# Kernel optimization log

Hardware: AMD Instinct MI355X
Metric: run time of the kernel (lower is better)

The kernel has to match this reference:

```python
import jax, jax.numpy as jnp
import numpy as np

NUM_HEADS = 16
EPS = 1e-6
CHUNK = 128  # chunk length for exact chunked-recurrent causal linear attention


def setup_inputs() -> dict:
    key = jax.random.key(0)
    ks = jax.random.split(key, 6)
    B, T, E = 4, 2048, 1024
    s = 0.02
    x = jax.random.normal(ks[0], (B, T, E), jnp.float32)
    Wq = jax.random.normal(ks[1], (E, E), jnp.float32) * s
    Wk = jax.random.normal(ks[2], (E, E), jnp.float32) * s
    Wv = jax.random.normal(ks[3], (E, E), jnp.float32) * s
    Wp = jax.random.normal(ks[4], (E, E), jnp.float32) * s
    bp = jnp.zeros((E,), jnp.float32)
    return {"x": x, "Wq": Wq, "Wk": Wk, "Wv": Wv, "Wp": Wp, "bp": bp}


def reference(x, Wq, Wk, Wv, Wp, bp):
    B, T, E = x.shape
    H = NUM_HEADS
    D = E // H
    N = T // CHUNK

    q = x @ Wq.T
    k = x @ Wk.T
    v = x @ Wv.T

    def split_heads(t):  # [B,T,E] -> [B,H,N,C,D]
        return t.reshape(B, T, H, D).transpose(0, 2, 1, 3).reshape(B, H, N, CHUNK, D)

    phi_q = jax.nn.elu(split_heads(q)) + 1.0
    phi_k = jax.nn.elu(split_heads(k)) + 1.0
    vh = split_heads(v)

    # per-chunk KV state and key-sum, then exclusive prefix over chunks
    kv = jnp.einsum('bhncd,bhnce->bhnde', phi_k, vh)        # [B,H,N,D,D]
    zk = phi_k.sum(axis=3)                                   # [B,H,N,D]
    S_prev = jnp.concatenate(
        [jnp.zeros_like(kv[:, :, :1]), jnp.cumsum(kv, axis=2)[:, :, :-1]], axis=2)
    Z_prev = jnp.concatenate(
        [jnp.zeros_like(zk[:, :, :1]), jnp.cumsum(zk, axis=2)[:, :, :-1]], axis=2)

    # intra-chunk causal part
    A = jnp.einsum('bhncd,bhnsd->bhncs', phi_q, phi_k)       # [B,H,N,C,C]
    mask = jnp.tril(jnp.ones((CHUNK, CHUNK), bool))
    A = jnp.where(mask, A, 0.0)

    num = (jnp.einsum('bhncs,bhnse->bhnce', A, vh)
           + jnp.einsum('bhncd,bhnde->bhnce', phi_q, S_prev))
    den = A.sum(-1) + jnp.einsum('bhncd,bhnd->bhnc', phi_q, Z_prev) + EPS
    y = num / den[..., None]                                  # [B,H,N,C,D]

    y = y.reshape(B, H, T, D).transpose(0, 2, 1, 3).reshape(B, T, E)
    return y @ Wp.T + bp
```

## Files before the change

### kernel.cpp

```cpp
#include <hip/hip_runtime.h>
#include <hip/hip_bf16.h>
#include <stdint.h>

#define T_LEN  2048
#define E_DIM  1024
#define BATCH  4
#define HEADS  16
#define HDIM   64
#define CHUNK_ 128
#define NCHUNK 16
#define EPS_   1e-6f

typedef __attribute__((ext_vector_type(8))) short bf16x8;
typedef __attribute__((ext_vector_type(4))) float f32x4;

__device__ __forceinline__ float b2f(__hip_bfloat16 h) { return __bfloat162float(h); }
__device__ __forceinline__ unsigned short f2bu(float f) {
  __hip_bfloat16 h = __float2bfloat16(f);
  return *(unsigned short*)&h;
}
__device__ __forceinline__ float bs2f(short v) {
  union { unsigned int u; float f; } c;
  c.u = ((unsigned int)(unsigned short)v) << 16;
  return c.f;
}
__device__ __forceinline__ void gld_lds16(const void* g, void* l) {
  __builtin_amdgcn_global_load_lds((const __attribute__((address_space(1))) void*)g,
                                   (__attribute__((address_space(3))) void*)l,
                                   16, 0, 0);
}

__global__ __launch_bounds__(256)
void cast5(const float* __restrict__ x,  const float* __restrict__ w0,
           const float* __restrict__ w1, const float* __restrict__ w2,
           const float* __restrict__ w3,
           __hip_bfloat16* __restrict__ xb,  __hip_bfloat16* __restrict__ w0b,
           __hip_bfloat16* __restrict__ w1b, __hip_bfloat16* __restrict__ w2b,
           __hip_bfloat16* __restrict__ w3b)
{
  const int b = blockIdx.x;
  const float* s;
  __hip_bfloat16* d;
  size_t off;
  if (b < 8192) { s = x; d = xb; off = (size_t)b * 1024; }
  else {
    const int i = (b - 8192) >> 10;
    const int r = (b - 8192) & 1023;
    s = (i == 0) ? w0 : (i == 1) ? w1 : (i == 2) ? w2 : w3;
    d = (i == 0) ? w0b : (i == 1) ? w1b : (i == 2) ? w2b : w3b;
    off = (size_t)r * 1024;
  }
  const int t = threadIdx.x;
  float4 v = *(const float4*)(s + off + (size_t)t * 4);
  ushort4 o;
  o.x = f2bu(v.x); o.y = f2bu(v.y); o.z = f2bu(v.z); o.w = f2bu(v.w);
  *(ushort4*)((unsigned short*)d + off + (size_t)t * 4) = o;
}

__device__ __forceinline__ void gemm128_core(
    const __hip_bfloat16* __restrict__ X,
    const __hip_bfloat16* __restrict__ W,
    int bm, int bn, f32x4 acc[4][4],
    __hip_bfloat16* Xs, __hip_bfloat16* Ws)
{
  const int t = threadIdx.x, lane = t & 63, wave = t >> 6;
  const int wm = (wave >> 1) * 64, wn = (wave & 1) * 64;
  for (int k0 = 0; k0 < 1024; k0 += 32) {
    if (k0) __syncthreads();
#pragma unroll
    for (int i = 0; i < 2; ++i) {
      const int j = wave * 2 + i;
      const int m = j * 16 + (lane >> 2);
      const int kg = lane & 3;
      gld_lds16(X + (size_t)(bm * 128 + m) * 1024 + k0 + kg * 8, (char*)Xs + j * 1024);
      gld_lds16(W + (size_t)(bn * 128 + m) * 1024 + k0 + kg * 8, (char*)Ws + j * 1024);
    }
    __syncthreads();
    bf16x8 a[4], b[4];
#pragma unroll
    for (int i = 0; i < 4; ++i) {
      a[i] = *(const bf16x8*)&Xs[((wm + i * 16 + (lane & 15)) * 4 + (lane >> 4)) * 8];
      b[i] = *(const bf16x8*)&Ws[((wn + i * 16 + (lane & 15)) * 4 + (lane >> 4)) * 8];
    }
#pragma unroll
    for (int i = 0; i < 4; ++i)
#pragma unroll
      for (int jn = 0; jn < 4; ++jn)
        acc[i][jn] = __builtin_amdgcn_mfma_f32_16x16x32_bf16(a[i], b[jn], acc[i][jn], 0, 0, 0);
  }
}

__global__ __launch_bounds__(256, 2)
void gemm_qkv(const __hip_bfloat16* __restrict__ X,
              const __hip_bfloat16* __restrict__ Wq,
              const __hip_bfloat16* __restrict__ Wk,
              const __hip_bfloat16* __restrict__ Wv,
              __hip_bfloat16* __restrict__ qo,
              __hip_bfloat16* __restrict__ ko,
              __hip_bfloat16* __restrict__ vo)
{
  __shared__ __align__(16) __hip_bfloat16 Xs[128 * 32];
  __shared__ __align__(16) __hip_bfloat16 Ws[128 * 32];
  const int bm = blockIdx.x, bnx = blockIdx.y;
  const int which = bnx >> 3, bn = bnx & 7;
  const __hip_bfloat16* W = (which == 0) ? Wq : (which == 1) ? Wk : Wv;
  __hip_bfloat16* C = (which == 0) ? qo : (which == 1) ? ko : vo;
  const bool elu = (which < 2);
  f32x4 acc[4][4];
#pragma unroll
  for (int i = 0; i < 4; ++i)
#pragma unroll
    for (int j = 0; j < 4; ++j) acc[i][j] = (f32x4){0.f, 0.f, 0.f, 0.f};
  gemm128_core(X, W, bm, bn, acc, Xs, Ws);
  const int lane = threadIdx.x & 63, wave = threadIdx.x >> 6;
  const int wm = (wave >> 1) * 64, wn = (wave & 1) * 64;
  const int r0 = (lane >> 4) * 4;
#pragma unroll
  for (int mi = 0; mi < 4; ++mi)
#pragma unroll
    for (int ni = 0; ni < 4; ++ni) {
      const int row = bm * 128 + wm + mi * 16 + r0;
      const int col = bn * 128 + wn + ni * 16 + (lane & 15);
#pragma unroll
      for (int r = 0; r < 4; ++r) {
        float v = acc[mi][ni][r];
        if (elu) v = (v > 0.f) ? (v + 1.f) : __expf(v);
        C[(size_t)(row + r) * 1024 + col] = __float2bfloat16(v);
      }
    }
}

__global__ __launch_bounds__(256, 2)
void gemm_out(const __hip_bfloat16* __restrict__ X,
              const __hip_bfloat16* __restrict__ W,
              const float* __restrict__ bias,
              float* __restrict__ C)
{
  __shared__ __align__(16) __hip_bfloat16 Xs[128 * 32];
  __shared__ __align__(16) __hip_bfloat16 Ws[128 * 32];
  const int bm = blockIdx.x, bn = blockIdx.y;
  f32x4 acc[4][4];
#pragma unroll
  for (int i = 0; i < 4; ++i)
#pragma unroll
    for (int j = 0; j < 4; ++j) acc[i][j] = (f32x4){0.f, 0.f, 0.f, 0.f};
  gemm128_core(X, W, bm, bn, acc, Xs, Ws);
  const int lane = threadIdx.x & 63, wave = threadIdx.x >> 6;
  const int wm = (wave >> 1) * 64, wn = (wave & 1) * 64;
  const int r0 = (lane >> 4) * 4;
#pragma unroll
  for (int mi = 0; mi < 4; ++mi)
#pragma unroll
    for (int ni = 0; ni < 4; ++ni) {
      const int row = bm * 128 + wm + mi * 16 + r0;
      const int col = bn * 128 + wn + ni * 16 + (lane & 15);
      const float bv = bias[col];
#pragma unroll
      for (int r = 0; r < 4; ++r)
        C[(size_t)(row + r) * 1024 + col] = acc[mi][ni][r] + bv;
    }
}

__global__ __launch_bounds__(256)
void chunk_kv(const __hip_bfloat16* __restrict__ Kp,
              const __hip_bfloat16* __restrict__ Vp,
              float* __restrict__ kvout, float* __restrict__ zkout)
{
  const int bid = blockIdx.x;
  const int n = bid & 15, h = (bid >> 4) & 15, b = bid >> 8;
  __shared__ __align__(16) __hip_bfloat16 ks[CHUNK_ * HDIM];
  __shared__ __align__(16) __hip_bfloat16 vs[CHUNK_ * HDIM];
  const size_t base = ((size_t)(b * T_LEN + n * CHUNK_)) * E_DIM + h * HDIM;
  const int t = threadIdx.x;
  for (int i = t; i < CHUNK_ * 8; i += 256) {
    int r = i >> 3, c = (i & 7) << 3;
    *(uint4*)&ks[r * HDIM + c] = *(const uint4*)(Kp + base + (size_t)r * E_DIM + c);
    *(uint4*)&vs[r * HDIM + c] = *(const uint4*)(Vp + base + (size_t)r * E_DIM + c);
  }
  __syncthreads();
  const int d0 = (t >> 4) << 2, e0 = (t & 15) << 2;
  float acc[4][4] = {{0.f}};
  float z[4] = {0.f, 0.f, 0.f, 0.f};
  for (int c = 0; c < CHUNK_; ++c) {
    float kv4[4], vv4[4];
#pragma unroll
    for (int i = 0; i < 4; ++i) kv4[i] = b2f(ks[c * HDIM + d0 + i]);
#pragma unroll
    for (int j = 0; j < 4; ++j) vv4[j] = b2f(vs[c * HDIM + e0 + j]);
#pragma unroll
    for (int i = 0; i < 4; ++i) {
      z[i] += kv4[i];
#pragma unroll
      for (int j = 0; j < 4; ++j) acc[i][j] += kv4[i] * vv4[j];
    }
  }
  float* o = kvout + (size_t)bid * (HDIM * HDIM);
#pragma unroll
  for (int i = 0; i < 4; ++i)
#pragma unroll
    for (int j = 0; j < 4; ++j)
      o[(e0 + j) * HDIM + (d0 + i)] = acc[i][j];
  if (e0 == 0) {
#pragma unroll
    for (int i = 0; i < 4; ++i) zkout[(size_t)bid * HDIM + d0 + i] = z[i];
  }
}

__global__ __launch_bounds__(256)
void prefix_chunks(float* __restrict__ S, float* __restrict__ Z)
{
  const int bh = blockIdx.x;
  const int t = threadIdx.x;
  float run[16];
#pragma unroll
  for (int j = 0; j < 16; ++j) run[j] = 0.f;
  for (int n = 0; n < NCHUNK; ++n) {
    float* p = S + ((size_t)bh * NCHUNK + n) * (HDIM * HDIM);
#pragma unroll
    for (int j = 0; j < 16; ++j) {
      int idx = t + j * 256;
      float cur = p[idx];
      p[idx] = run[j];
      run[j] += cur;
    }
  }
  if (t < HDIM) {
    float rz = 0.f;
    for (int n = 0; n < NCHUNK; ++n) {
      float* p = Z + ((size_t)bh * NCHUNK + n) * HDIM + t;
      float cur = *p;
      *p = rz;
      rz += cur;
    }
  }
}

__global__ __launch_bounds__(256, 2)
void chunk_attn(const __hip_bfloat16* __restrict__ Qp,
                const __hip_bfloat16* __restrict__ Kp,
                const __hip_bfloat16* __restrict__ Vp,
                const float* __restrict__ STp,
                const float* __restrict__ Zp,
                __hip_bfloat16* __restrict__ Yp)
{
  __shared__ __align__(16) __hip_bfloat16 QK[16384];
  __shared__ __align__(16) __hip_bfloat16 Vt[8192];
  __shared__ __align__(16) __hip_bfloat16 Sb[4096];
  __shared__ float den_lds[128];
  __shared__ float Zs[64];

  const int bid = blockIdx.x;
  const int n = bid & 15, h = (bid >> 4) & 15, b = bid >> 8;
  const int tokbase = b * T_LEN + n * CHUNK_;
  const size_t gbase = (size_t)tokbase * E_DIM + h * HDIM;
  const int t = threadIdx.x, lane = t & 63, wv = t >> 6;
  unsigned short* QKu = (unsigned short*)QK;
  short* VtS = (short*)Vt;

#pragma unroll
  for (int i = 0; i < 4; ++i) {
    const int m = i * 32 + (t >> 3);
    const int d0 = (t & 7) << 3;
    uint4 qv = *(const uint4*)(Qp + gbase + (size_t)m * E_DIM + d0);
    uint4 kv = *(const uint4*)(Kp + gbase + (size_t)m * E_DIM + d0);
    *(uint4*)&QK[((d0 >> 3) * 128 + m) * 8] = qv;
    *(uint4*)&QK[8192 + ((d0 >> 3) * 128 + m) * 8] = kv;
  }
#pragma unroll
  for (int i = 0; i < 4; ++i) {
    const int j = wv * 4 + i;
    const int slot = j * 64 + lane;
    const int s = slot >> 3, e8 = slot & 7;
    gld_lds16(Vp + gbase + (size_t)s * E_DIM + e8 * 8, (char*)Vt + j * 1024);
  }
  {
    const float* Sg = STp + (size_t)bid * (HDIM * HDIM);
    const int e = t >> 2, quad = t & 3;
#pragma unroll
    for (int i = 0; i < 4; ++i) {
      const int d0 = quad * 16 + i * 4;
      float4 sv = *(const float4*)(Sg + e * HDIM + d0);
      ushort4 o;
      o.x = f2bu(sv.x); o.y = f2bu(sv.y); o.z = f2bu(sv.z); o.w = f2bu(sv.w);
      *(ushort4*)&QKu[0] ;
      *(ushort4*)&((unsigned short*)Sb)[((d0 >> 3) * 64 + e) * 8 + (d0 & 7)] = o;
    }
  }
  if (t < 64) Zs[t] = Zp[(size_t)bid * HDIM + t];
  __syncthreads();

  const int mts[2] = { wv, 7 - wv };
  f32x4 accn[2][4];
#pragma unroll
  for (int i = 0; i < 2; ++i)
#pragma unroll
    for (int j = 0; j < 4; ++j) accn[i][j] = (f32x4){0.f, 0.f, 0.f, 0.f};

#pragma unroll
  for (int mi = 0; mi < 2; ++mi) {
    const int m0 = mts[mi] * 16;
#pragma unroll
    for (int kh = 0; kh < 2; ++kh) {
      bf16x8 a = *(const bf16x8*)&QK[(((kh * 4) + (lane >> 4)) * 128 + m0 + (lane & 15)) * 8];
#pragma unroll
      for (int ne = 0; ne < 4; ++ne) {
        bf16x8 bsf = *(const bf16x8*)&Sb[(((kh * 4) + (lane >> 4)) * 64 + ne * 16 + (lane & 15)) * 8];
        accn[mi][ne] = __builtin_amdgcn_mfma_f32_16x16x32_bf16(a, bsf, accn[mi][ne], 0, 0, 0);
      }
    }
  }
  if (t < 128) {
    float dn = EPS_;
#pragma unroll
    for (int kg = 0; kg < 8; ++kg) {
      bf16x8 qv = *(const bf16x8*)&QK[(kg * 128 + t) * 8];
#pragma unroll
      for (int j = 0; j < 8; ++j) dn += bs2f(qv[j]) * Zs[kg * 8 + j];
    }
    den_lds[t] = dn;
  }
  uint2 packP[9];
  {
    int np = 0;
#pragma unroll
    for (int mi = 0; mi < 2; ++mi) {
      const int mt = mts[mi], m0 = mt * 16;
      bf16x8 aq0 = *(const bf16x8*)&QK[(((lane >> 4)) * 128 + m0 + (lane & 15)) * 8];
      bf16x8 aq1 = *(const bf16x8*)&QK[((4 + (lane >> 4)) * 128 + m0 + (lane & 15)) * 8];
      for (int nt = 0; nt <= mt; ++nt) {
        f32x4 acc = (f32x4){0.f, 0.f, 0.f, 0.f};
        bf16x8 b0 = *(const bf16x8*)&QK[8192 + (((lane >> 4)) * 128 + nt * 16 + (lane & 15)) * 8];
        bf16x8 b1 = *(const bf16x8*)&QK[8192 + ((4 + (lane >> 4)) * 128 + nt * 16 + (lane & 15)) * 8];
        acc = __builtin_amdgcn_mfma_f32_16x16x32_bf16(aq0, b0, acc, 0, 0, 0);
        acc = __builtin_amdgcn_mfma_f32_16x16x32_bf16(aq1, b1, acc, 0, 0, 0);
        unsigned short u[4];
#pragma unroll
        for (int r = 0; r < 4; ++r) {
          float v = acc[r];
          if (nt == mt) {
            const bool keep = (lane & 15) <= (((lane >> 4) * 4) + r);
            v = keep ? v : 0.f;
          }
          u[r] = f2bu(v);
        }
        packP[np].x = (unsigned)u[0] | ((unsigned)u[1] << 16);
        packP[np].y = (unsigned)u[2] | ((unsigned)u[3] << 16);
        ++np;
      }
    }
  }
  __syncthreads();

  {
    int np = 0;
#pragma unroll
    for (int mi = 0; mi < 2; ++mi) {
      const int mt = mts[mi], m0 = mt * 16;
      for (int nt = 0; nt <= mt; ++nt) {
        const uint2 p = packP[np++];
        const int s = nt * 16 + (lane & 15);
        const int kgs = s >> 3, se = s & 7;
#pragma unroll
        for (int r = 0; r < 4; ++r) {
          const int m = m0 + (lane >> 4) * 4 + r;
          unsigned short us = (r < 2) ? (unsigned short)(p.x >> (r * 16))
                                      : (unsigned short)(p.y >> ((r - 2) * 16));
          QKu[(kgs * 128 + m) * 8 + se] = us;
        }
      }
      if ((mt & 1) == 0 && lane < 32) {
        const int slot = (2 * mt + 2 + (lane >> 4)) * 128 + m0 + (lane & 15);
        *(uint4*)&QK[slot * 8] = (uint4){0u, 0u, 0u, 0u};
      }
    }
  }
  __syncthreads();

  bf16x8 ones;
#pragma unroll
  for (int j = 0; j < 8; ++j) ones[j] = (short)0x3F80;
  f32x4 accden[2];
  accden[0] = (f32x4){0.f, 0.f, 0.f, 0.f};
  accden[1] = (f32x4){0.f, 0.f, 0.f, 0.f};
#pragma unroll
  for (int mi = 0; mi < 2; ++mi) {
    const int mt = mts[mi], m0 = mt * 16;
    const int ktc = (mt + 2) >> 1;
    for (int kt = 0; kt < ktc; ++kt) {
      bf16x8 a = *(const bf16x8*)&QK[((kt * 4 + (lane >> 4)) * 128 + m0 + (lane & 15)) * 8];
      accden[mi] = __builtin_amdgcn_mfma_f32_16x16x32_bf16(a, ones, accden[mi], 0, 0, 0);
#pragma unroll
      for (int ne = 0; ne < 4; ++ne) {
        bf16x8 bv;
#pragma unroll
        for (int j = 0; j < 8; ++j)
          bv[j] = VtS[(kt * 32 + (lane >> 4) * 8 + j) * 64 + ne * 16 + (lane & 15)];
        accn[mi][ne] = __builtin_amdgcn_mfma_f32_16x16x32_bf16(a, bv, accn[mi][ne], 0, 0, 0);
      }
    }
    if ((lane & 15) == 0) {
#pragma unroll
      for (int r = 0; r < 4; ++r)
        den_lds[m0 + (lane >> 4) * 4 + r] += accden[mi][r];
    }
  }
  __syncthreads();

#pragma unroll
  for (int mi = 0; mi < 2; ++mi) {
    const int m0 = mts[mi] * 16;
    float inv[4];
#pragma unroll
    for (int r = 0; r < 4; ++r)
      inv[r] = 1.f / den_lds[m0 + (lane >> 4) * 4 + r];
#pragma unroll
    for (int ne = 0; ne < 4; ++ne) {
      const int col = h * HDIM + ne * 16 + (lane & 15);
#pragma unroll
      for (int r = 0; r < 4; ++r) {
        const int row = tokbase + m0 + (lane >> 4) * 4 + r;
        Yp[(size_t)row * E_DIM + col] = __float2bfloat16(accn[mi][ne][r] * inv[r]);
      }
    }
  }
}

extern "C" void kernel_launch(void* const* d_in, const int* in_sizes, int n_in,
                              void* d_out, int out_size, void* d_ws, size_t ws_size,
                              hipStream_t stream)
{
  const float* x  = (const float*)d_in[0];
  const float* Wq = (const float*)d_in[1];
  const float* Wk = (const float*)d_in[2];
  const float* Wv = (const float*)d_in[3];
  const float* Wp = (const float*)d_in[4];
  const float* bp = (const float*)d_in[5];
  float* out = (float*)d_out;

  const size_t MT = (size_t)BATCH * T_LEN;
  char* w = (char*)d_ws;
  __hip_bfloat16* xb  = (__hip_bfloat16*)w; w += MT * E_DIM * sizeof(__hip_bfloat16);
  __hip_bfloat16* Wqb = (__hip_bfloat16*)w; w += (size_t)E_DIM * E_DIM * sizeof(__hip_bfloat16);
  __hip_bfloat16* Wkb = (__hip_bfloat16*)w; w += (size_t)E_DIM * E_DIM * sizeof(__hip_bfloat16);
  __hip_bfloat16* Wvb = (__hip_bfloat16*)w; w += (size_t)E_DIM * E_DIM * sizeof(__hip_bfloat16);
  __hip_bfloat16* Wpb = (__hip_bfloat16*)w; w += (size_t)E_DIM * E_DIM * sizeof(__hip_bfloat16);
  __hip_bfloat16* q = (__hip_bfloat16*)w; w += MT * E_DIM * sizeof(__hip_bfloat16);
  __hip_bfloat16* k = (__hip_bfloat16*)w; w += MT * E_DIM * sizeof(__hip_bfloat16);
  __hip_bfloat16* v = (__hip_bfloat16*)w; w += MT * E_DIM * sizeof(__hip_bfloat16);
  __hip_bfloat16* y = (__hip_bfloat16*)w; w += MT * E_DIM * sizeof(__hip_bfloat16);
  float* S = (float*)w; w += (size_t)BATCH * HEADS * NCHUNK * HDIM * HDIM * sizeof(float);
  float* Z = (float*)w; w += (size_t)BATCH * HEADS * NCHUNK * HDIM * sizeof(float);

  cast5<<<8192 + 4096, 256, 0, stream>>>(x, Wq, Wk, Wv, Wp, xb, Wqb, Wkb, Wvb, Wpb);
  gemm_qkv<<<dim3(MT / 128, 24), 256, 0, stream>>>(xb, Wqb, Wkb, Wvb, q, k, v);
  chunk_kv<<<BATCH * HEADS * NCHUNK, 256, 0, stream>>>(k, v, S, Z);
  prefix_chunks<<<BATCH * HEADS, 256, 0, stream>>>(S, Z);
  chunk_attn<<<BATCH * HEADS * NCHUNK, 256, 0, stream>>>(q, k, v, S, Z, y);
  gemm_out<<<dim3(MT / 128, 8), 256, 0, stream>>>(y, Wpb, bp, out);
}
```

Baseline: 256.2 us.

## Restructure chunk attention with pre-packed V/S layouts and per-wave P tiles

chunk_kv now writes the KV state directly in the MFMA-friendly blocked layout and also emits a pre-transposed bf16 V image (reusing the xb buffer), so chunk_attn can load V and S with straight vector copies instead of gathering. chunk_attn keeps Q fragments in registers loaded directly from global, computes the denominator with an MFMA against Z, and stores each wave's masked QK^T tile in a private padded LDS region instead of rewriting a shared QK buffer, which removes two block barriers. LDS use shrinks and launch bounds allow three blocks per CU. The cost is that K fragments are now read from global inside the inner loop and chunk_kv does extra transpose writes.

```diff
diff --git a/kernel.cpp b/kernel.cpp
--- a/kernel.cpp
+++ b/kernel.cpp
@@ -18,11 +18,6 @@
 __device__ __forceinline__ unsigned short f2bu(float f) {
   __hip_bfloat16 h = __float2bfloat16(f);
   return *(unsigned short*)&h;
-}
-__device__ __forceinline__ float bs2f(short v) {
-  union { unsigned int u; float f; } c;
-  c.u = ((unsigned int)(unsigned short)v) << 16;
-  return c.f;
 }
 __device__ __forceinline__ void gld_lds16(const void* g, void* l) {
   __builtin_amdgcn_global_load_lds((const __attribute__((address_space(1))) void*)g,
@@ -164,7 +159,8 @@
 __global__ __launch_bounds__(256)
 void chunk_kv(const __hip_bfloat16* __restrict__ Kp,
               const __hip_bfloat16* __restrict__ Vp,
-              float* __restrict__ kvout, float* __restrict__ zkout)
+              float* __restrict__ kvout, float* __restrict__ zkout,
+              unsigned short* __restrict__ vimg)
 {
   const int bid = blockIdx.x;
   const int n = bid & 15, h = (bid >> 4) & 15, b = bid >> 8;
@@ -195,14 +191,27 @@
     }
   }
   float* o = kvout + (size_t)bid * (HDIM * HDIM);
+  const int dg = d0 >> 3, doff = d0 & 7;
 #pragma unroll
   for (int i = 0; i < 4; ++i)
 #pragma unroll
     for (int j = 0; j < 4; ++j)
-      o[(e0 + j) * HDIM + (d0 + i)] = acc[i][j];
+      o[dg * 512 + (e0 + j) * 8 + doff + i] = acc[i][j];
   if (e0 == 0) {
 #pragma unroll
     for (int i = 0; i < 4; ++i) zkout[(size_t)bid * HDIM + d0 + i] = z[i];
+  }
+  const unsigned short* vsu = (const unsigned short*)vs;
+  unsigned short* vo = vimg + (size_t)bid * 8192;
+  for (int slot = t; slot < 1024; slot += 256) {
+    const int sg = slot >> 6, e = slot & 63;
+    ushort4 lo, hi;
+    lo.x = vsu[(sg * 8 + 0) * 64 + e]; lo.y = vsu[(sg * 8 + 1) * 64 + e];
+    lo.z = vsu[(sg * 8 + 2) * 64 + e]; lo.w = vsu[(sg * 8 + 3) * 64 + e];
+    hi.x = vsu[(sg * 8 + 4) * 64 + e]; hi.y = vsu[(sg * 8 + 5) * 64 + e];
+    hi.z = vsu[(sg * 8 + 6) * 64 + e]; hi.w = vsu[(sg * 8 + 7) * 64 + e];
+    *(ushort4*)&vo[slot * 8] = lo;
+    *(ushort4*)&vo[slot * 8 + 4] = hi;
   }
 }
 
@@ -235,190 +244,142 @@
   }
 }
 
-__global__ __launch_bounds__(256, 2)
+#define PW_STRIDE 136
+
+__global__ __launch_bounds__(256, 3)
 void chunk_attn(const __hip_bfloat16* __restrict__ Qp,
                 const __hip_bfloat16* __restrict__ Kp,
-                const __hip_bfloat16* __restrict__ Vp,
-                const float* __restrict__ STp,
+                const unsigned short* __restrict__ vimg,
+                const float* __restrict__ Simg,
                 const float* __restrict__ Zp,
                 __hip_bfloat16* __restrict__ Yp)
 {
-  __shared__ __align__(16) __hip_bfloat16 QK[16384];
-  __shared__ __align__(16) __hip_bfloat16 Vt[8192];
-  __shared__ __align__(16) __hip_bfloat16 Sb[4096];
-  __shared__ float den_lds[128];
-  __shared__ float Zs[64];
+  __shared__ __align__(16) unsigned short VL[8192];
+  __shared__ __align__(16) unsigned short SL[4096];
+  __shared__ __align__(16) unsigned short PL[4 * 16 * PW_STRIDE];
 
   const int bid = blockIdx.x;
   const int n = bid & 15, h = (bid >> 4) & 15, b = bid >> 8;
   const int tokbase = b * T_LEN + n * CHUNK_;
   const size_t gbase = (size_t)tokbase * E_DIM + h * HDIM;
   const int t = threadIdx.x, lane = t & 63, wv = t >> 6;
-  unsigned short* QKu = (unsigned short*)QK;
-  short* VtS = (short*)Vt;
-
-#pragma unroll
-  for (int i = 0; i < 4; ++i) {
-    const int m = i * 32 + (t >> 3);
-    const int d0 = (t & 7) << 3;
-    uint4 qv = *(const uint4*)(Qp + gbase + (size_t)m * E_DIM + d0);
-    uint4 kv = *(const uint4*)(Kp + gbase + (size_t)m * E_DIM + d0);
-    *(uint4*)&QK[((d0 >> 3) * 128 + m) * 8] = qv;
-    *(uint4*)&QK[8192 + ((d0 >> 3) * 128 + m) * 8] = kv;
-  }
+  const int lm = lane & 15, kg = lane >> 4;
+
 #pragma unroll
   for (int i = 0; i < 4; ++i) {
     const int j = wv * 4 + i;
-    const int slot = j * 64 + lane;
-    const int s = slot >> 3, e8 = slot & 7;
-    gld_lds16(Vp + gbase + (size_t)s * E_DIM + e8 * 8, (char*)Vt + j * 1024);
-  }
-  {
-    const float* Sg = STp + (size_t)bid * (HDIM * HDIM);
-    const int e = t >> 2, quad = t & 3;
-#pragma unroll
-    for (int i = 0; i < 4; ++i) {
-      const int d0 = quad * 16 + i * 4;
-      float4 sv = *(const float4*)(Sg + e * HDIM + d0);
-      ushort4 o;
-      o.x = f2bu(sv.x); o.y = f2bu(sv.y); o.z = f2bu(sv.z); o.w = f2bu(sv.w);
-      *(ushort4*)&QKu[0] ;
-      *(ushort4*)&((unsigned short*)Sb)[((d0 >> 3) * 64 + e) * 8 + (d0 & 7)] = o;
-    }
-  }
-  if (t < 64) Zs[t] = Zp[(size_t)bid * HDIM + t];
+    gld_lds16(vimg + (size_t)bid * 8192 + (size_t)(j * 64 + lane) * 8,
+              (char*)VL + j * 1024);
+  }
+#pragma unroll
+  for (int i = 0; i < 4; ++i) {
+    const int idx = i * 1024 + t * 4;
+    float4 s4 = *(const float4*)(Simg + (size_t)bid * 4096 + idx);
+    ushort4 o;
+    o.x = f2bu(s4.x); o.y = f2bu(s4.y); o.z = f2bu(s4.z); o.w = f2bu(s4.w);
+    *(ushort4*)&SL[idx] = o;
+  }
+
+  const int mts[2] = { wv, 7 - wv };
+  bf16x8 aq[2][2];
+#pragma unroll
+  for (int mi = 0; mi < 2; ++mi)
+#pragma unroll
+    for (int kh = 0; kh < 2; ++kh)
+      aq[mi][kh] = *(const bf16x8*)(Qp + gbase +
+                    (size_t)(mts[mi] * 16 + lm) * E_DIM + kh * 32 + kg * 8);
+  bf16x8 zb[2];
+#pragma unroll
+  for (int kh = 0; kh < 2; ++kh) {
+    float4 z0 = *(const float4*)(Zp + (size_t)bid * 64 + kh * 32 + kg * 8);
+    float4 z1 = *(const float4*)(Zp + (size_t)bid * 64 + kh * 32 + kg * 8 + 4);
+    zb[kh][0] = (short)f2bu(z0.x); zb[kh][1] = (short)f2bu(z0.y);
+    zb[kh][2] = (short)f2bu(z0.z); zb[kh][3] = (short)f2bu(z0.w);
+    zb[kh][4] = (short)f2bu(z1.x); zb[kh][5] = (short)f2bu(z1.y);
+    zb[kh][6] = (short)f2bu(z1.z); zb[kh][7] = (short)f2bu(z1.w);
+  }
+
   __syncthreads();
 
-  const int mts[2] = { wv, 7 - wv };
   f32x4 accn[2][4];
-#pragma unroll
-  for (int i = 0; i < 2; ++i)
-#pragma unroll
-    for (int j = 0; j < 4; ++j) accn[i][j] = (f32x4){0.f, 0.f, 0.f, 0.f};
-
+  f32x4 accden[2];
 #pragma unroll
   for (int mi = 0; mi < 2; ++mi) {
-    const int m0 = mts[mi] * 16;
+    accden[mi] = (f32x4){EPS_, EPS_, EPS_, EPS_};
+#pragma unroll
+    for (int ne = 0; ne < 4; ++ne) accn[mi][ne] = (f32x4){0.f, 0.f, 0.f, 0.f};
+  }
+
+#pragma unroll
+  for (int mi = 0; mi < 2; ++mi)
 #pragma unroll
     for (int kh = 0; kh < 2; ++kh) {
-      bf16x8 a = *(const bf16x8*)&QK[(((kh * 4) + (lane >> 4)) * 128 + m0 + (lane & 15)) * 8];
+      const bf16x8 a = aq[mi][kh];
+      accden[mi] = __builtin_amdgcn_mfma_f32_16x16x32_bf16(a, zb[kh], accden[mi], 0, 0, 0);
 #pragma unroll
       for (int ne = 0; ne < 4; ++ne) {
-        bf16x8 bsf = *(const bf16x8*)&Sb[(((kh * 4) + (lane >> 4)) * 64 + ne * 16 + (lane & 15)) * 8];
-        accn[mi][ne] = __builtin_amdgcn_mfma_f32_16x16x32_bf16(a, bsf, accn[mi][ne], 0, 0, 0);
-      }
-    }
-  }
-  if (t < 128) {
-    float dn = EPS_;
-#pragma unroll
-    for (int kg = 0; kg < 8; ++kg) {
-      bf16x8 qv = *(const bf16x8*)&QK[(kg * 128 + t) * 8];
-#pragma unroll
-      for (int j = 0; j < 8; ++j) dn += bs2f(qv[j]) * Zs[kg * 8 + j];
-    }
-    den_lds[t] = dn;
-  }
-  uint2 packP[9];
-  {
-    int np = 0;
-#pragma unroll
-    for (int mi = 0; mi < 2; ++mi) {
-      const int mt = mts[mi], m0 = mt * 16;
-      bf16x8 aq0 = *(const bf16x8*)&QK[(((lane >> 4)) * 128 + m0 + (lane & 15)) * 8];
-      bf16x8 aq1 = *(const bf16x8*)&QK[((4 + (lane >> 4)) * 128 + m0 + (lane & 15)) * 8];
-      for (int nt = 0; nt <= mt; ++nt) {
-        f32x4 acc = (f32x4){0.f, 0.f, 0.f, 0.f};
-        bf16x8 b0 = *(const bf16x8*)&QK[8192 + (((lane >> 4)) * 128 + nt * 16 + (lane & 15)) * 8];
-        bf16x8 b1 = *(const bf16x8*)&QK[8192 + ((4 + (lane >> 4)) * 128 + nt * 16 + (lane & 15)) * 8];
-        acc = __builtin_amdgcn_mfma_f32_16x16x32_bf16(aq0, b0, acc, 0, 0, 0);
-        acc = __builtin_amdgcn_mfma_f32_16x16x32_bf16(aq1, b1, acc, 0, 0, 0);
-        unsigned short u[4];
-#pragma unroll
-        for (int r = 0; r < 4; ++r) {
-          float v = acc[r];
-          if (nt == mt) {
-            const bool keep = (lane & 15) <= (((lane >> 4) * 4) + r);
-            v = keep ? v : 0.f;
-          }
-          u[r] = f2bu(v);
-        }
-        packP[np].x = (unsigned)u[0] | ((unsigned)u[1] << 16);
-        packP[np].y = (unsigned)u[2] | ((unsigned)u[3] << 16);
-        ++np;
-      }
-    }
-  }
-  __syncthreads();
-
-  {
-    int np = 0;
-#pragma unroll
-    for (int mi = 0; mi < 2; ++mi) {
-      const int mt = mts[mi], m0 = mt * 16;
-      for (int nt = 0; nt <= mt; ++nt) {
-        const uint2 p = packP[np++];
-        const int s = nt * 16 + (lane & 15);
-        const int kgs = s >> 3, se = s & 7;
-#pragma unroll
-        for (int r = 0; r < 4; ++r) {
-          const int m = m0 + (lane >> 4) * 4 + r;
-          unsigned short us = (r < 2) ? (unsigned short)(p.x >> (r * 16))
-                                      : (unsigned short)(p.y >> ((r - 2) * 16));
-          QKu[(kgs * 128 + m) * 8 + se] = us;
-        }
-      }
-      if ((mt & 1) == 0 && lane < 32) {
-        const int slot = (2 * mt + 2 + (lane >> 4)) * 128 + m0 + (lane & 15);
-        *(uint4*)&QK[slot * 8] = (uint4){0u, 0u, 0u, 0u};
-      }
-    }
-  }
-  __syncthreads();
-
+        bf16x8 bs = *(const bf16x8*)&SL[((kh * 4 + kg) * 64 + ne * 16 + lm) * 8];
+        accn[mi][ne] = __builtin_amdgcn_mfma_f32_16x16x32_bf16(a, bs, accn[mi][ne], 0, 0, 0);
+      }
+    }
+
+  unsigned short* Pw = PL + wv * 16 * PW_STRIDE;
   bf16x8 ones;
 #pragma unroll
   for (int j = 0; j < 8; ++j) ones[j] = (short)0x3F80;
-  f32x4 accden[2];
-  accden[0] = (f32x4){0.f, 0.f, 0.f, 0.f};
-  accden[1] = (f32x4){0.f, 0.f, 0.f, 0.f};
+
 #pragma unroll
   for (int mi = 0; mi < 2; ++mi) {
     const int mt = mts[mi], m0 = mt * 16;
+    for (int nt = 0; nt <= mt; ++nt) {
+      f32x4 pt = (f32x4){0.f, 0.f, 0.f, 0.f};
+#pragma unroll
+      for (int kh = 0; kh < 2; ++kh) {
+        bf16x8 ak = *(const bf16x8*)(Kp + gbase +
+                     (size_t)(nt * 16 + lm) * E_DIM + kh * 32 + kg * 8);
+        pt = __builtin_amdgcn_mfma_f32_16x16x32_bf16(ak, aq[mi][kh], pt, 0, 0, 0);
+      }
+      unsigned short u[4];
+#pragma unroll
+      for (int r = 0; r < 4; ++r) {
+        float v = pt[r];
+        if (nt == mt) {
+          v = ((kg * 4 + r) <= lm) ? v : 0.f;
+        }
+        u[r] = f2bu(v);
+      }
+      const int sidx = lm * PW_STRIDE + nt * 16 + kg * 4;
+      *(unsigned*)&Pw[sidx]     = (unsigned)u[0] | ((unsigned)u[1] << 16);
+      *(unsigned*)&Pw[sidx + 2] = (unsigned)u[2] | ((unsigned)u[3] << 16);
+    }
+    if ((mt & 1) == 0 && lane < 32) {
+      const int m = lane >> 1, half = lane & 1;
+      *(uint4*)&Pw[m * PW_STRIDE + (mt + 1) * 16 + half * 8] = (uint4){0u, 0u, 0u, 0u};
+    }
     const int ktc = (mt + 2) >> 1;
     for (int kt = 0; kt < ktc; ++kt) {
-      bf16x8 a = *(const bf16x8*)&QK[((kt * 4 + (lane >> 4)) * 128 + m0 + (lane & 15)) * 8];
-      accden[mi] = __builtin_amdgcn_mfma_f32_16x16x32_bf16(a, ones, accden[mi], 0, 0, 0);
+      bf16x8 ap = *(const bf16x8*)&Pw[lm * PW_STRIDE + kt * 32 + kg * 8];
+      accden[mi] = __builtin_amdgcn_mfma_f32_16x16x32_bf16(ap, ones, accden[mi], 0, 0, 0);
 #pragma unroll
       for (int ne = 0; ne < 4; ++ne) {
-        bf16x8 bv;
-#pragma unroll
-        for (int j = 0; j < 8; ++j)
-          bv[j] = VtS[(kt * 32 + (lane >> 4) * 8 + j) * 64 + ne * 16 + (lane & 15)];
-        accn[mi][ne] = __builtin_amdgcn_mfma_f32_16x16x32_bf16(a, bv, accn[mi][ne], 0, 0, 0);
-      }
-    }
-    if ((lane & 15) == 0) {
-#pragma unroll
-      for (int r = 0; r < 4; ++r)
-        den_lds[m0 + (lane >> 4) * 4 + r] += accden[mi][r];
-    }
-  }
-  __syncthreads();
+        bf16x8 bv = *(const bf16x8*)&VL[((kt * 4 + kg) * 64 + ne * 16 + lm) * 8];
+        accn[mi][ne] = __builtin_amdgcn_mfma_f32_16x16x32_bf16(ap, bv, accn[mi][ne], 0, 0, 0);
+      }
+    }
+  }
 
 #pragma unroll
   for (int mi = 0; mi < 2; ++mi) {
     const int m0 = mts[mi] * 16;
     float inv[4];
 #pragma unroll
-    for (int r = 0; r < 4; ++r)
-      inv[r] = 1.f / den_lds[m0 + (lane >> 4) * 4 + r];
+    for (int r = 0; r < 4; ++r) inv[r] = 1.f / accden[mi][r];
 #pragma unroll
     for (int ne = 0; ne < 4; ++ne) {
-      const int col = h * HDIM + ne * 16 + (lane & 15);
+      const int col = h * HDIM + ne * 16 + lm;
 #pragma unroll
       for (int r = 0; r < 4; ++r) {
-        const int row = tokbase + m0 + (lane >> 4) * 4 + r;
+        const int row = tokbase + m0 + kg * 4 + r;
         Yp[(size_t)row * E_DIM + col] = __float2bfloat16(accn[mi][ne][r] * inv[r]);
       }
     }
@@ -450,11 +411,12 @@
   __hip_bfloat16* y = (__hip_bfloat16*)w; w += MT * E_DIM * sizeof(__hip_bfloat16);
   float* S = (float*)w; w += (size_t)BATCH * HEADS * NCHUNK * HDIM * HDIM * sizeof(float);
   float* Z = (float*)w; w += (size_t)BATCH * HEADS * NCHUNK * HDIM * sizeof(float);
+  unsigned short* vimg = (unsigned short*)xb;
 
   cast5<<<8192 + 4096, 256, 0, stream>>>(x, Wq, Wk, Wv, Wp, xb, Wqb, Wkb, Wvb, Wpb);
   gemm_qkv<<<dim3(MT / 128, 24), 256, 0, stream>>>(xb, Wqb, Wkb, Wvb, q, k, v);
-  chunk_kv<<<BATCH * HEADS * NCHUNK, 256, 0, stream>>>(k, v, S, Z);
+  chunk_kv<<<BATCH * HEADS * NCHUNK, 256, 0, stream>>>(k, v, S, Z, vimg);
   prefix_chunks<<<BATCH * HEADS, 256, 0, stream>>>(S, Z);
-  chunk_attn<<<BATCH * HEADS * NCHUNK, 256, 0, stream>>>(q, k, v, S, Z, y);
+  chunk_attn<<<BATCH * HEADS * NCHUNK, 256, 0, stream>>>(q, k, vimg, S, Z, y);
   gemm_out<<<dim3(MT / 128, 8), 256, 0, stream>>>(y, Wpb, bp, out);
 }
```

Result: faster. 246.6 us (median of 2 runs) (-3.8%).
